# Performance work log

Measured on AMD Instinct MI355X. Metric: run time of the kernel, lower is better.

Reference implementation:

```python
import jax, jax.numpy as jnp
import numpy as np
import math

B, S, D, H = 2, 2048, 1024, 16
D_K = D // H


def setup_inputs() -> dict:
    key = jax.random.key(0)
    ks = jax.random.split(key, 9)
    scale = 0.02
    return {
        "query": jax.random.normal(ks[0], (B, S, D), dtype=jnp.float32),
        "key": jax.random.normal(ks[1], (B, S, D), dtype=jnp.float32),
        "value": jax.random.normal(ks[2], (B, S, D), dtype=jnp.float32),
        "padding_mask": jax.random.bernoulli(ks[3], 0.1, (B, 1, 1, S)),
        "Wq": jax.random.normal(ks[4], (D, D), dtype=jnp.float32) * scale,
        "bq": jnp.zeros((D,), dtype=jnp.float32),
        "Wk": jax.random.normal(ks[5], (D, D), dtype=jnp.float32) * scale,
        "bk": jnp.zeros((D,), dtype=jnp.float32),
        "Wv": jax.random.normal(ks[6], (D, D), dtype=jnp.float32) * scale,
        "bv": jnp.zeros((D,), dtype=jnp.float32),
        "Wo": jax.random.normal(ks[7], (D, D), dtype=jnp.float32) * scale,
        "bo": jnp.zeros((D,), dtype=jnp.float32),
    }


def reference(query, key, value, padding_mask, Wq, bq, Wk, bk, Wv, bv, Wo, bo):
    # projections -> [B, H, S, d_k]
    q = (query @ Wq + bq).reshape(B, S, H, D_K).transpose(0, 2, 1, 3)
    k = (key @ Wk + bk).reshape(B, S, H, D_K).transpose(0, 2, 1, 3)
    v = (value @ Wv + bv).reshape(B, S, H, D_K).transpose(0, 2, 1, 3)

    # scores: [B, H, S, S]
    scores = jnp.einsum("bhqd,bhkd->bhqk", q, k) / math.sqrt(D_K)

    # faithful to original: triu(scores, 1).bool() -> True where upper-tri score != 0,
    # masked positions get value 1e-10 (NOT -inf) before softmax
    causal_mask = jnp.triu(scores, k=1) != 0
    scores = jnp.where(causal_mask, jnp.float32(1e-10), scores)
    scores = jnp.where(padding_mask, jnp.float32(1e-10), scores)

    attn = jax.nn.softmax(scores, axis=-1)
    out = jnp.einsum("bhqk,bhkd->bhqd", attn, v)  # [B, H, S, d_k]
    out = out.transpose(0, 2, 1, 3).reshape(B, S, D)
    return out @ Wo + bo
```

## Files before the change

### kernel.cpp

```cpp
#include <hip/hip_runtime.h>
#include <hip/hip_bf16.h>
#include <cstdint>
#include <cstddef>

typedef __hip_bfloat16 bf16;
typedef __attribute__((ext_vector_type(8))) short short8;
typedef __attribute__((ext_vector_type(4))) short s4v;
typedef __attribute__((ext_vector_type(4))) float floatx4;

#define B_ 2
#define S_ 2048
#define D_ 1024
#define H_ 16
#define DK_ 64
#define M_ 4096
#define HEADELEMS 131072
#define TILEELEMS 4096
#define QSCALE 0.1803368801111204f

struct __align__(8) bf16x4 { bf16 x, y, z, w; };

__device__ __forceinline__ floatx4 mfma16(short8 a, short8 b, floatx4 c) {
  return __builtin_amdgcn_mfma_f32_16x16x32_bf16(a, b, c, 0, 0, 0);
}
__device__ __forceinline__ void gl_lds16(const bf16* g, bf16* l) {
  __builtin_amdgcn_global_load_lds((const __attribute__((address_space(1))) void*)g,
                                   (__attribute__((address_space(3))) void*)l, 16, 0, 0);
}
__device__ __forceinline__ float bs2f(short s) {
  bf16 b = *reinterpret_cast<bf16*>(&s);
  return __bfloat162float(b);
}
__device__ __forceinline__ s4v pack4(float p0, float p1, float p2, float p3) {
  union { __hip_bfloat162 h; short2 s; } ua, ub;
  ua.h = __float22bfloat162_rn(make_float2(p0, p1));
  ub.h = __float22bfloat162_rn(make_float2(p2, p3));
  s4v r = {ua.s.x, ua.s.y, ub.s.x, ub.s.y};
  return r;
}
__device__ __forceinline__ float fast_exp2(float x) {
#if __has_builtin(__builtin_amdgcn_exp2f)
  return __builtin_amdgcn_exp2f(x);
#else
  float r; asm("v_exp_f32 %0, %1" : "=v"(r) : "v"(x)); return r;
#endif
}

__global__ void prep_kernel(const float* __restrict__ q_in, const float* __restrict__ k_in,
                            const float* __restrict__ v_in,
                            const float* __restrict__ Wq, const float* __restrict__ Wk,
                            const float* __restrict__ Wv, const float* __restrict__ Wo,
                            bf16* __restrict__ xq, bf16* __restrict__ xk, bf16* __restrict__ xv,
                            bf16* __restrict__ wqt, bf16* __restrict__ wkt,
                            bf16* __restrict__ wvt, bf16* __restrict__ wot,
                            const unsigned int* __restrict__ pmask, int* __restrict__ flag) {
  __shared__ bf16 tile[64][66];
  __shared__ int sbyte;
  const int blk = blockIdx.x;
  const int tid = threadIdx.x;
  if (blk < 12288) {
    const int z = blk >> 12;
    const int i = ((blk & 4095) << 8) | tid;
    const float* src = (z == 0) ? q_in : (z == 1) ? k_in : v_in;
    bf16* dst = (z == 0) ? xq : (z == 1) ? xk : xv;
    float4 v = ((const float4*)src)[i];
    bf16x4 o = { __float2bfloat16(v.x), __float2bfloat16(v.y),
                 __float2bfloat16(v.z), __float2bfloat16(v.w) };
    ((bf16x4*)dst)[i] = o;
  } else if (blk < 13312) {
    const int t = blk - 12288;
    const int z = t >> 8;
    const int rc = t & 255;
    const int r0 = (rc >> 4) * 64, c0 = (rc & 15) * 64;
    const float* src = (z == 0) ? Wq : (z == 1) ? Wk : (z == 2) ? Wv : Wo;
    bf16* dst = (z == 0) ? wqt : (z == 1) ? wkt : (z == 2) ? wvt : wot;
    const int lr = tid >> 4;
    const int lc4 = (tid & 15) * 4;
#pragma unroll
    for (int i = 0; i < 4; ++i) {
      const int r = lr + i * 16;
      float4 v = *(const float4*)(src + (size_t)(r0 + r) * D_ + c0 + lc4);
      tile[r][lc4 + 0] = __float2bfloat16(v.x);
      tile[r][lc4 + 1] = __float2bfloat16(v.y);
      tile[r][lc4 + 2] = __float2bfloat16(v.z);
      tile[r][lc4 + 3] = __float2bfloat16(v.w);
    }
    __syncthreads();
    const int orr = tid & 63;
    const int oc0 = tid >> 6;
#pragma unroll
    for (int j = 0; j < 16; ++j) {
      const int oc = oc0 + j * 4;
      dst[(size_t)(c0 + oc) * D_ + r0 + orr] = tile[orr][oc];
    }
  } else {
    if (tid == 0) sbyte = 0;
    __syncthreads();
    for (int i = tid; i < (B_ * S_) / 4; i += 256) {
      const unsigned int v = pmask[i];
      if (((v & 0xFEFEFEFEu) == 0u) && ((v & 0xFFFFFF00u) != 0u)) sbyte = 1;
    }
    __syncthreads();
    if (tid == 0) *flag = sbyte;
  }
}

template<int MT>
__global__ __launch_bounds__(256, 2) void gemm_k(
    const bf16* __restrict__ A0, const bf16* __restrict__ A1, const bf16* __restrict__ A2,
    const bf16* __restrict__ W0, const bf16* __restrict__ W1, const bf16* __restrict__ W2,
    const float* __restrict__ b0, const float* __restrict__ b1, const float* __restrict__ b2,
    void* __restrict__ O0, void* __restrict__ O1, void* __restrict__ O2,
    const int mode01, const int Kd, const float sc)
{
  __shared__ __align__(16) bf16 sh[(MT + 128) * 32];
  bf16* As = sh;
  bf16* Bs = sh + MT * 32;
  const int z = blockIdx.z;
  const bf16* A = (z == 0) ? A0 : (z == 1) ? A1 : A2;
  const bf16* W = (z == 0) ? W0 : (z == 1) ? W1 : W2;
  const float* bias = (z == 0) ? b0 : (z == 1) ? b1 : b2;
  void* Cout = (z == 0) ? O0 : (z == 1) ? O1 : O2;
  const int mode = (z == 2) ? 1 : mode01;
  const float scz = (z == 0) ? sc : 1.f;

  constexpr int MI = MT / 32;
  const int tid = threadIdx.x;
  const int wave = tid >> 6, lane = tid & 63;
  const int quad = lane >> 4, lc = lane & 15;
  const int wm = (wave >> 1) * (MT / 2), wn = (wave & 1) * 64;
  const int m0 = blockIdx.y * MT, n0 = blockIdx.x * 128;

  const floatx4 zero4 = {0.f, 0.f, 0.f, 0.f};
  floatx4 acc[MI][4];
#pragma unroll
  for (int mi = 0; mi < MI; ++mi)
#pragma unroll
    for (int ni = 0; ni < 4; ++ni) acc[mi][ni] = zero4;

  const int ldr = lane >> 2;
  const int ldc = (lane & 3) * 8;
  const bf16* Ag = A + (size_t)(m0 + wave * (MT / 4) + ldr) * Kd + ldc;
  const bf16* Bg = W + (size_t)(n0 + wave * 32 + ldr) * Kd + ldc;
  bf16* As0 = As + wave * (MT / 4) * 32;
  bf16* Bs0 = Bs + wave * 32 * 32;

  for (int k0 = 0; k0 < Kd; k0 += 32) {
    gl_lds16(Ag + k0, As0);
    if (MT == 128) gl_lds16(Ag + k0 + (size_t)16 * Kd, As0 + 16 * 32);
    gl_lds16(Bg + k0, Bs0);
    gl_lds16(Bg + k0 + (size_t)16 * Kd, Bs0 + 16 * 32);
    __syncthreads();

    short8 af[MI], bfr[4];
#pragma unroll
    for (int i = 0; i < MI; ++i)
      af[i] = *(const short8*)(As + (wm + i * 16 + lc) * 32 + quad * 8);
#pragma unroll
    for (int i = 0; i < 4; ++i)
      bfr[i] = *(const short8*)(Bs + (wn + i * 16 + lc) * 32 + quad * 8);
#pragma unroll
    for (int mi = 0; mi < MI; ++mi)
#pragma unroll
      for (int ni = 0; ni < 4; ++ni)
        acc[mi][ni] = mfma16(af[mi], bfr[ni], acc[mi][ni]);
    __syncthreads();
  }

  if (mode == 2) {
    float* out = (float*)Cout;
#pragma unroll
    for (int mi = 0; mi < MI; ++mi)
#pragma unroll
      for (int ni = 0; ni < 4; ++ni) {
        const int col = n0 + wn + ni * 16 + lc;
        const float bv = bias[col];
        const int rbase = m0 + wm + mi * 16 + quad * 4;
#pragma unroll
        for (int r = 0; r < 4; ++r)
          out[(size_t)(rbase + r) * D_ + col] = acc[mi][ni][r] + bv;
      }
  } else {
    bf16* pool = sh + wave * 2048;
    float bvs[4];
#pragma unroll
    for (int ni = 0; ni < 4; ++ni) bvs[ni] = bias[n0 + wn + ni * 16 + lc];
    const int hcol = (n0 + wn) >> 6;
    const int mglob = m0 + wm;
    bf16* outb = (bf16*)Cout + (size_t)((mglob >> 11) * H_ + hcol) * HEADELEMS
               + (size_t)((mglob & (S_ - 1)) >> 6) * TILEELEMS;
#pragma unroll
    for (int half = 0; half < MI / 2; ++half) {
#pragma unroll
      for (int mi2 = 0; mi2 < 2; ++mi2) {
        const int mi = half * 2 + mi2;
#pragma unroll
        for (int ni = 0; ni < 4; ++ni) {
          const int dkl = ni * 16 + lc;
#pragma unroll
          for (int r = 0; r < 4; ++r) {
            const float v = (acc[mi][ni][r] + bvs[ni]) * scz;
            int idx;
            if (mode == 0) {
              const int c = (mi2 * 2 + (dkl >> 5)) * 64 + ((dkl >> 3) & 3) * 16 + quad * 4 + r;
              idx = c * 8 + (dkl & 7);
            } else {
              const int c = (mi2 * 4 + (dkl >> 4)) * 64 + quad * 16 + (dkl & 15);
              idx = c * 4 + r;
            }
            pool[idx] = __float2bfloat16(v);
          }
        }
      }
#pragma unroll
      for (int t = 0; t < 4; ++t) {
        const short8 vv = *(const short8*)(pool + t * 512 + lane * 8);
        *(short8*)(outb + half * 2048 + t * 512 + lane * 8) = vv;
      }
    }
  }
}

__global__ void suf_kernel(const bf16* __restrict__ vp, float* __restrict__ suf) {
  __shared__ float ts[32 * 64];
  const int bhid = blockIdx.x;
  const bf16* vb = vp + (size_t)bhid * HEADELEMS;
  const int tid = threadIdx.x;
  const int dk = tid & 63, g = tid >> 6;
  const int dkt = dk >> 4, lck = dk & 15;
  for (int T = g * 8; T < g * 8 + 8; ++T) {
    float sum = 0.f;
#pragma unroll
    for (int w = 0; w < 4; ++w)
#pragma unroll
      for (int qd = 0; qd < 4; ++qd) {
        const s4v x = *(const s4v*)(vb + (size_t)T * TILEELEMS
                                    + (size_t)(((w * 4 + dkt) * 64 + qd * 16 + lck)) * 4);
        sum += bs2f(x[0]) + bs2f(x[1]) + bs2f(x[2]) + bs2f(x[3]);
      }
    ts[T * 64 + dk] = sum;
  }
  __syncthreads();
  if (g == 0) {
    float run = 0.f;
    float* out = suf + (size_t)bhid * (33 * 64);
    out[32 * 64 + dk] = 0.f;
    for (int T = 31; T >= 0; --T) { run += ts[T * 64 + dk]; out[T * 64 + dk] = run; }
  }
}

__device__ __forceinline__ void load_pad(const void* pad, int bytemode, int idx, bool pm[4]) {
  if (bytemode) {
    const uchar4 u = *(const uchar4*)((const unsigned char*)pad + idx);
    pm[0] = u.x != 0; pm[1] = u.y != 0; pm[2] = u.z != 0; pm[3] = u.w != 0;
  } else {
    const int4 u = *(const int4*)((const int*)pad + idx);
    pm[0] = u.x != 0; pm[1] = u.y != 0; pm[2] = u.z != 0; pm[3] = u.w != 0;
  }
}

struct KVF {
  short8 ak00, ak01, ak10, ak11;
  s4v va0[4], va1[4];
  bool pm0[4], pm1[4];
};

__device__ __forceinline__ void load_kv(const bf16* kwp, const bf16* vwp,
                                        const void* pad, const int bytemode,
                                        const int pidx, const int p, KVF& f) {
  const size_t o0 = (size_t)(2 * p) * TILEELEMS, o1 = o0 + TILEELEMS;
  f.ak00 = *(const short8*)(kwp + o0);
  f.ak01 = *(const short8*)(kwp + o0 + 512);
  f.ak10 = *(const short8*)(kwp + o1);
  f.ak11 = *(const short8*)(kwp + o1 + 512);
#pragma unroll
  for (int dkt = 0; dkt < 4; ++dkt) {
    f.va0[dkt] = *(const s4v*)(vwp + o0 + dkt * 256);
    f.va1[dkt] = *(const s4v*)(vwp + o1 + dkt * 256);
  }
  load_pad(pad, bytemode, pidx + 2 * p * 64, f.pm0);
  load_pad(pad, bytemode, pidx + (2 * p + 1) * 64, f.pm1);
}

template<bool DIAGP>
__device__ __forceinline__ void qk_tile(const short8 ak0, const short8 ak1,
                                        const short8 (&qf)[4][2],
                                        const bool pm[4], float (&lacc)[4], s4v (&pf)[4],
                                        const int w, const int quad, const int lc,
                                        const bool diag) {
  const floatx4 z4 = {0.f, 0.f, 0.f, 0.f};
  const short ONE = (short)0x3F80;
#pragma unroll
  for (int qt = 0; qt < 4; ++qt) {
    if (DIAGP && diag && w > qt) {
      s4v o1 = {ONE, ONE, ONE, ONE};
      pf[qt] = o1;
      lacc[qt] += 4.f;
      continue;
    }
    floatx4 s = mfma16(ak0, qf[qt][0], z4);
    s = mfma16(ak1, qf[qt][1], s);
    float pv[4];
#pragma unroll
    for (int r = 0; r < 4; ++r) {
      bool m = pm[r];
      if (DIAGP && diag && w == qt) m = m || (quad * 4 + r > lc);
      pv[r] = fast_exp2(m ? 0.f : s[r]);
      lacc[qt] += pv[r];
    }
    pf[qt] = pack4(pv[0], pv[1], pv[2], pv[3]);
  }
}

__device__ __forceinline__ void pv_step(const KVF& f, const s4v (&pf0)[4], const s4v (&pf1)[4],
                                        floatx4 (&oacc)[4][4]) {
  short8 pB[4];
#pragma unroll
  for (int qt = 0; qt < 4; ++qt)
    pB[qt] = __builtin_shufflevector(pf0[qt], pf1[qt], 0, 1, 2, 3, 4, 5, 6, 7);
#pragma unroll
  for (int dkt = 0; dkt < 4; ++dkt) {
    const short8 av = __builtin_shufflevector(f.va0[dkt], f.va1[dkt], 0, 1, 2, 3, 4, 5, 6, 7);
#pragma unroll
    for (int qt = 0; qt < 4; ++qt)
      oacc[dkt][qt] = mfma16(av, pB[qt], oacc[dkt][qt]);
  }
}

__global__ __launch_bounds__(256, 1) void attn_kernel(
    const bf16* __restrict__ qp, const bf16* __restrict__ kp,
    const bf16* __restrict__ vp, const float* __restrict__ suf,
    const void* __restrict__ pad, const int* __restrict__ flag,
    bf16* __restrict__ oa)
{
  __shared__ __align__(16) bf16 smem[13312];
  __shared__ float lbuf[256];

  const int lin = blockIdx.x;
  const int xcd = lin & 7;
  const int t = lin >> 3;
  const int grp = t >> 4;
  const int jq = t & 15;
  const int bh = xcd + 8 * grp;
  const int b = bh >> 4, h = bh & 15;

  const int tid = threadIdx.x;
  const int w = tid >> 6, lane = tid & 63, quad = lane >> 4, lc = lane & 15;
  const int bytemode = *flag;
  const int pidx = b * S_ + w * 16 + quad * 4;

  const bf16* kwp = kp + (size_t)bh * HEADELEMS + (size_t)(w * 128 + lane) * 8;
  const bf16* vwp = vp + (size_t)bh * HEADELEMS + (size_t)(w * 4 * 64 + lane) * 4;

#pragma unroll 1
  for (int qsel = 0; qsel < 2; ++qsel) {
    const int myqt = qsel ? jq : 31 - jq;
    const int mynt = myqt + 1;
    const int pfull = (mynt - 1) >> 1;

    const bf16* qb = qp + (size_t)bh * HEADELEMS + (size_t)myqt * TILEELEMS;
    short8 qf[4][2];
#pragma unroll
    for (int qt = 0; qt < 4; ++qt)
#pragma unroll
      for (int hh = 0; hh < 2; ++hh)
        qf[qt][hh] = *(const short8*)(qb + (size_t)((qt * 2 + hh) * 64 + lane) * 8);

    const floatx4 zero4 = {0.f, 0.f, 0.f, 0.f};
    floatx4 oacc[4][4];
#pragma unroll
    for (int i = 0; i < 4; ++i)
#pragma unroll
      for (int jj = 0; jj < 4; ++jj) oacc[i][jj] = zero4;
    float lacc[4] = {0.f, 0.f, 0.f, 0.f};

    KVF f;
    load_kv(kwp, vwp, pad, bytemode, pidx, 0, f);
#pragma unroll 1
    for (int p = 0; p < pfull; ++p) {
      KVF fn;
      load_kv(kwp, vwp, pad, bytemode, pidx, p + 1, fn);
      s4v pf0[4], pf1[4];
      qk_tile<false>(f.ak00, f.ak01, qf, f.pm0, lacc, pf0, w, quad, lc, false);
      qk_tile<false>(f.ak10, f.ak11, qf, f.pm1, lacc, pf1, w, quad, lc, false);
      pv_step(f, pf0, pf1, oacc);
      f = fn;
    }
    {
      const int T0 = 2 * pfull, T1 = T0 + 1;
      s4v pf0[4], pf1[4];
      qk_tile<true>(f.ak00, f.ak01, qf, f.pm0, lacc, pf0, w, quad, lc, T0 == mynt - 1);
      if (T1 < mynt) {
        qk_tile<true>(f.ak10, f.ak11, qf, f.pm1, lacc, pf1, w, quad, lc, T1 == mynt - 1);
      } else {
        const s4v zz = {0, 0, 0, 0};
#pragma unroll
        for (int qt = 0; qt < 4; ++qt) pf1[qt] = zz;
      }
      pv_step(f, pf0, pf1, oacc);
    }

#pragma unroll
    for (int qt = 0; qt < 4; ++qt) {
      float v = lacc[qt];
      v += __shfl_xor(v, 16);
      v += __shfl_xor(v, 32);
      if (quad == 0) lbuf[w * 64 + qt * 16 + lc] = v;
    }
    __syncthreads();
    float* fbuf = (float*)smem;
    bf16* obuf = smem + 8704;
    float ls = lbuf[0 * 64 + w * 16 + lc] + lbuf[1 * 64 + w * 16 + lc]
             + lbuf[2 * 64 + w * 16 + lc] + lbuf[3 * 64 + w * 16 + lc];
    ls += (float)(S_ - mynt * 64);
    const float linv = 1.f / ls;
    const float* sufp = suf + (size_t)bh * (33 * 64) + mynt * 64;

#pragma unroll
    for (int dktG = 0; dktG < 4; ++dktG) {
#pragma unroll
      for (int qt = 0; qt < 4; ++qt) {
        const floatx4 a = oacc[dktG][qt];
        float* dst = fbuf + (w * 4 + qt) * 272 + lc;
#pragma unroll
        for (int r = 0; r < 4; ++r) dst[(quad * 4 + r) * 17] = a[r];
      }
      __syncthreads();
      const float4 sv4 = *(const float4*)(sufp + dktG * 16 + quad * 4);
      float v[4];
#pragma unroll
      for (int r = 0; r < 4; ++r) {
        const int e = (quad * 4 + r) * 17 + lc;
        v[r] = fbuf[(0 * 4 + w) * 272 + e] + fbuf[(1 * 4 + w) * 272 + e]
             + fbuf[(2 * 4 + w) * 272 + e] + fbuf[(3 * 4 + w) * 272 + e];
      }
      v[0] = (v[0] + sv4.x) * linv; v[1] = (v[1] + sv4.y) * linv;
      v[2] = (v[2] + sv4.z) * linv; v[3] = (v[3] + sv4.w) * linv;
      bf16x4 pk = { __float2bfloat16(v[0]), __float2bfloat16(v[1]),
                    __float2bfloat16(v[2]), __float2bfloat16(v[3]) };
      *(bf16x4*)(obuf + (w * 16 + lc) * 72 + dktG * 16 + quad * 4) = pk;
      __syncthreads();
    }

    const size_t obase = (size_t)(b * S_ + myqt * 64) * D_ + h * 64;
#pragma unroll
    for (int it = 0; it < 2; ++it) {
      const int idx = it * 256 + tid;
      const int row = idx >> 3, c8 = (idx & 7) * 8;
      const short8 vv = *(const short8*)(obuf + row * 72 + c8);
      *(short8*)(oa + obase + (size_t)row * D_ + c8) = vv;
    }
  }
}

extern "C" void kernel_launch(void* const* d_in, const int* in_sizes, int n_in,
                              void* d_out, int out_size, void* d_ws, size_t ws_size,
                              hipStream_t stream) {
  (void)in_sizes; (void)n_in; (void)out_size; (void)ws_size;
  const float* q_in = (const float*)d_in[0];
  const float* k_in = (const float*)d_in[1];
  const float* v_in = (const float*)d_in[2];
  const void*  pmask = d_in[3];
  const float* Wq = (const float*)d_in[4];
  const float* bq = (const float*)d_in[5];
  const float* Wk = (const float*)d_in[6];
  const float* bk = (const float*)d_in[7];
  const float* Wv = (const float*)d_in[8];
  const float* bv = (const float*)d_in[9];
  const float* Wo = (const float*)d_in[10];
  const float* bo = (const float*)d_in[11];

  char* ws = (char*)d_ws;
  bf16* xq  = (bf16*)(ws + 0);
  bf16* xk  = (bf16*)(ws + 8388608);
  bf16* xv  = (bf16*)(ws + 16777216);
  bf16* wqt = (bf16*)(ws + 25165824);
  bf16* wkt = (bf16*)(ws + 27262976);
  bf16* wvt = (bf16*)(ws + 29360128);
  bf16* wot = (bf16*)(ws + 31457280);
  bf16* qpp = (bf16*)(ws + 33554432);
  bf16* kpp = (bf16*)(ws + 41943040);
  bf16* vpp = (bf16*)(ws + 50331648);
  float* suf = (float*)(ws + 25165824);
  int*  flg = (int*)(ws + 58720256);
  bf16* oa  = xq;

  prep_kernel<<<13313, 256, 0, stream>>>(q_in, k_in, v_in, Wq, Wk, Wv, Wo,
                                         xq, xk, xv, wqt, wkt, wvt, wot,
                                         (const unsigned int*)pmask, flg);

  gemm_k<128><<<dim3(8, 32, 3), 256, 0, stream>>>(xq, xk, xv, wqt, wkt, wvt,
                                                  bq, bk, bv, qpp, kpp, vpp, 0, D_, QSCALE);
  suf_kernel<<<32, 256, 0, stream>>>(vpp, suf);

  attn_kernel<<<512, 256, 0, stream>>>(qpp, kpp, vpp, suf, pmask, flg, oa);

  gemm_k<64><<<dim3(8, 64, 1), 256, 0, stream>>>(oa, oa, oa, wot, wot, wot,
                                                 bo, bo, bo, d_out, d_out, d_out, 2, D_, 1.f);
}
```

Before: 249.7 us.

## Stage K/V tiles through double-buffered LDS with async loads and bitmask padding

Replaces the register-prefetched K/V loads in the attention loop with asynchronous global-to-LDS copies into two ping-pong buffers. Each wave waits only on its own outstanding loads with vmcnt before reading its slice back from LDS. The padding mask is read once per block and packed into per-lane 32-bit masks, so the per-tile mask loads disappear. The goal is to cut register pressure and better hide memory latency. The cost is a larger LDS footprint, extra LDS reads, and extra barriers around the epilogue.

```diff
diff --git a/kernel.cpp b/kernel.cpp
--- a/kernel.cpp
+++ b/kernel.cpp
@@ -249,43 +249,11 @@
   }
 }
 
-__device__ __forceinline__ void load_pad(const void* pad, int bytemode, int idx, bool pm[4]) {
-  if (bytemode) {
-    const uchar4 u = *(const uchar4*)((const unsigned char*)pad + idx);
-    pm[0] = u.x != 0; pm[1] = u.y != 0; pm[2] = u.z != 0; pm[3] = u.w != 0;
-  } else {
-    const int4 u = *(const int4*)((const int*)pad + idx);
-    pm[0] = u.x != 0; pm[1] = u.y != 0; pm[2] = u.z != 0; pm[3] = u.w != 0;
-  }
-}
-
-struct KVF {
-  short8 ak00, ak01, ak10, ak11;
-  s4v va0[4], va1[4];
-  bool pm0[4], pm1[4];
-};
-
-__device__ __forceinline__ void load_kv(const bf16* kwp, const bf16* vwp,
-                                        const void* pad, const int bytemode,
-                                        const int pidx, const int p, KVF& f) {
-  const size_t o0 = (size_t)(2 * p) * TILEELEMS, o1 = o0 + TILEELEMS;
-  f.ak00 = *(const short8*)(kwp + o0);
-  f.ak01 = *(const short8*)(kwp + o0 + 512);
-  f.ak10 = *(const short8*)(kwp + o1);
-  f.ak11 = *(const short8*)(kwp + o1 + 512);
-#pragma unroll
-  for (int dkt = 0; dkt < 4; ++dkt) {
-    f.va0[dkt] = *(const s4v*)(vwp + o0 + dkt * 256);
-    f.va1[dkt] = *(const s4v*)(vwp + o1 + dkt * 256);
-  }
-  load_pad(pad, bytemode, pidx + 2 * p * 64, f.pm0);
-  load_pad(pad, bytemode, pidx + (2 * p + 1) * 64, f.pm1);
-}
-
 template<bool DIAGP>
 __device__ __forceinline__ void qk_tile(const short8 ak0, const short8 ak1,
                                         const short8 (&qf)[4][2],
-                                        const bool pm[4], float (&lacc)[4], s4v (&pf)[4],
+                                        const unsigned int (&pmb)[4], const int T,
+                                        float (&lacc)[4], s4v (&pf)[4],
                                         const int w, const int quad, const int lc,
                                         const bool diag) {
   const floatx4 z4 = {0.f, 0.f, 0.f, 0.f};
@@ -303,7 +271,7 @@
     float pv[4];
 #pragma unroll
     for (int r = 0; r < 4; ++r) {
-      bool m = pm[r];
+      bool m = ((pmb[r] >> T) & 1u) != 0u;
       if (DIAGP && diag && w == qt) m = m || (quad * 4 + r > lc);
       pv[r] = fast_exp2(m ? 0.f : s[r]);
       lacc[qt] += pv[r];
@@ -312,7 +280,8 @@
   }
 }
 
-__device__ __forceinline__ void pv_step(const KVF& f, const s4v (&pf0)[4], const s4v (&pf1)[4],
+__device__ __forceinline__ void pv_step(const s4v (&va0)[4], const s4v (&va1)[4],
+                                        const s4v (&pf0)[4], const s4v (&pf1)[4],
                                         floatx4 (&oacc)[4][4]) {
   short8 pB[4];
 #pragma unroll
@@ -320,11 +289,28 @@
     pB[qt] = __builtin_shufflevector(pf0[qt], pf1[qt], 0, 1, 2, 3, 4, 5, 6, 7);
 #pragma unroll
   for (int dkt = 0; dkt < 4; ++dkt) {
-    const short8 av = __builtin_shufflevector(f.va0[dkt], f.va1[dkt], 0, 1, 2, 3, 4, 5, 6, 7);
+    const short8 av = __builtin_shufflevector(va0[dkt], va1[dkt], 0, 1, 2, 3, 4, 5, 6, 7);
 #pragma unroll
     for (int qt = 0; qt < 4; ++qt)
       oacc[dkt][qt] = mfma16(av, pB[qt], oacc[dkt][qt]);
   }
+}
+
+__device__ __forceinline__ void stage8(const bf16* kb, const bf16* vb, bf16* slot,
+                                       const int T0, const int T1,
+                                       const int wl, const int wreg) {
+  const bf16* k0 = kb + (size_t)T0 * TILEELEMS + wl;
+  const bf16* k1 = kb + (size_t)T1 * TILEELEMS + wl;
+  const bf16* v0 = vb + (size_t)T0 * TILEELEMS + wl;
+  const bf16* v1 = vb + (size_t)T1 * TILEELEMS + wl;
+  gl_lds16(k0,       slot + wreg);
+  gl_lds16(k0 + 512, slot + wreg + 512);
+  gl_lds16(k1,       slot + 4096 + wreg);
+  gl_lds16(k1 + 512, slot + 4096 + wreg + 512);
+  gl_lds16(v0,       slot + 8192 + wreg);
+  gl_lds16(v0 + 512, slot + 8192 + wreg + 512);
+  gl_lds16(v1,       slot + 12288 + wreg);
+  gl_lds16(v1 + 512, slot + 12288 + wreg + 512);
 }
 
 __global__ __launch_bounds__(256, 1) void attn_kernel(
@@ -333,8 +319,7 @@
     const void* __restrict__ pad, const int* __restrict__ flag,
     bf16* __restrict__ oa)
 {
-  __shared__ __align__(16) bf16 smem[13312];
-  __shared__ float lbuf[256];
+  __shared__ __align__(16) bf16 lds[32768];
 
   const int lin = blockIdx.x;
   const int xcd = lin & 7;
@@ -347,24 +332,57 @@
   const int tid = threadIdx.x;
   const int w = tid >> 6, lane = tid & 63, quad = lane >> 4, lc = lane & 15;
   const int bytemode = *flag;
-  const int pidx = b * S_ + w * 16 + quad * 4;
-
-  const bf16* kwp = kp + (size_t)bh * HEADELEMS + (size_t)(w * 128 + lane) * 8;
-  const bf16* vwp = vp + (size_t)bh * HEADELEMS + (size_t)(w * 4 * 64 + lane) * 4;
+
+  const int wreg = w * 1024;
+  const int wl = wreg + lane * 8;
+  const int vl = wreg + lane * 4;
+
+  const bf16* kb = kp + (size_t)bh * HEADELEMS;
+  const bf16* vb = vp + (size_t)bh * HEADELEMS;
+
+  unsigned int pmb[4] = {0u, 0u, 0u, 0u};
+  if (bytemode) {
+    const unsigned char* pp = (const unsigned char*)pad + b * S_ + w * 16 + quad * 4;
+#pragma unroll
+    for (int T = 0; T < 32; ++T) {
+      const uchar4 u = *(const uchar4*)(pp + T * 64);
+      pmb[0] |= (u.x ? 1u : 0u) << T;
+      pmb[1] |= (u.y ? 1u : 0u) << T;
+      pmb[2] |= (u.z ? 1u : 0u) << T;
+      pmb[3] |= (u.w ? 1u : 0u) << T;
+    }
+  } else {
+    const int* pp = (const int*)pad + b * S_ + w * 16 + quad * 4;
+#pragma unroll
+    for (int T = 0; T < 32; ++T) {
+      const int4 u = *(const int4*)(pp + (size_t)T * 64);
+      pmb[0] |= (u.x ? 1u : 0u) << T;
+      pmb[1] |= (u.y ? 1u : 0u) << T;
+      pmb[2] |= (u.z ? 1u : 0u) << T;
+      pmb[3] |= (u.w ? 1u : 0u) << T;
+    }
+  }
 
 #pragma unroll 1
   for (int qsel = 0; qsel < 2; ++qsel) {
     const int myqt = qsel ? jq : 31 - jq;
     const int mynt = myqt + 1;
-    const int pfull = (mynt - 1) >> 1;
+    const int np = (mynt + 1) >> 1;
 
     const bf16* qb = qp + (size_t)bh * HEADELEMS + (size_t)myqt * TILEELEMS;
+    gl_lds16(qb + wl,       lds + 16384 + wreg);
+    gl_lds16(qb + wl + 512, lds + 16384 + wreg + 512);
+    stage8(kb, vb, lds, 0, 1, wl, wreg);
+    asm volatile("s_waitcnt vmcnt(0)" ::: "memory");
+    __syncthreads();
+
     short8 qf[4][2];
 #pragma unroll
     for (int qt = 0; qt < 4; ++qt)
 #pragma unroll
       for (int hh = 0; hh < 2; ++hh)
-        qf[qt][hh] = *(const short8*)(qb + (size_t)((qt * 2 + hh) * 64 + lane) * 8);
+        qf[qt][hh] = *(const short8*)(lds + 16384 + qt * 1024 + hh * 512 + lane * 8);
+    __syncthreads();
 
     const floatx4 zero4 = {0.f, 0.f, 0.f, 0.f};
     floatx4 oacc[4][4];
@@ -374,31 +392,51 @@
       for (int jj = 0; jj < 4; ++jj) oacc[i][jj] = zero4;
     float lacc[4] = {0.f, 0.f, 0.f, 0.f};
 
-    KVF f;
-    load_kv(kwp, vwp, pad, bytemode, pidx, 0, f);
 #pragma unroll 1
-    for (int p = 0; p < pfull; ++p) {
-      KVF fn;
-      load_kv(kwp, vwp, pad, bytemode, pidx, p + 1, fn);
+    for (int p = 0; p < np; ++p) {
+      if (p + 1 < np) {
+        stage8(kb, vb, lds + (((p + 1) & 1) << 14), 2 * p + 2, 2 * p + 3, wl, wreg);
+        asm volatile("s_waitcnt vmcnt(8)" ::: "memory");
+      } else {
+        asm volatile("s_waitcnt vmcnt(0)" ::: "memory");
+      }
+      __builtin_amdgcn_sched_barrier(0);
+
+      bf16* slot = lds + ((p & 1) << 14);
+      const short8 ak00 = *(const short8*)(slot + wl);
+      const short8 ak01 = *(const short8*)(slot + wl + 512);
+      const short8 ak10 = *(const short8*)(slot + 4096 + wl);
+      const short8 ak11 = *(const short8*)(slot + 4096 + wl + 512);
+      s4v va0[4], va1[4];
+#pragma unroll
+      for (int dkt = 0; dkt < 4; ++dkt) {
+        va0[dkt] = *(const s4v*)(slot + 8192 + vl + dkt * 256);
+        va1[dkt] = *(const s4v*)(slot + 12288 + vl + dkt * 256);
+      }
+
+      const int T0 = 2 * p, T1 = 2 * p + 1;
       s4v pf0[4], pf1[4];
-      qk_tile<false>(f.ak00, f.ak01, qf, f.pm0, lacc, pf0, w, quad, lc, false);
-      qk_tile<false>(f.ak10, f.ak11, qf, f.pm1, lacc, pf1, w, quad, lc, false);
-      pv_step(f, pf0, pf1, oacc);
-      f = fn;
-    }
-    {
-      const int T0 = 2 * pfull, T1 = T0 + 1;
-      s4v pf0[4], pf1[4];
-      qk_tile<true>(f.ak00, f.ak01, qf, f.pm0, lacc, pf0, w, quad, lc, T0 == mynt - 1);
-      if (T1 < mynt) {
-        qk_tile<true>(f.ak10, f.ak11, qf, f.pm1, lacc, pf1, w, quad, lc, T1 == mynt - 1);
+      if (p + 1 < np) {
+        qk_tile<false>(ak00, ak01, qf, pmb, T0, lacc, pf0, w, quad, lc, false);
+        qk_tile<false>(ak10, ak11, qf, pmb, T1, lacc, pf1, w, quad, lc, false);
       } else {
-        const s4v zz = {0, 0, 0, 0};
-#pragma unroll
-        for (int qt = 0; qt < 4; ++qt) pf1[qt] = zz;
-      }
-      pv_step(f, pf0, pf1, oacc);
-    }
+        qk_tile<true>(ak00, ak01, qf, pmb, T0, lacc, pf0, w, quad, lc, T0 == mynt - 1);
+        if (T1 < mynt) {
+          qk_tile<true>(ak10, ak11, qf, pmb, T1, lacc, pf1, w, quad, lc, true);
+        } else {
+          const s4v zz = {0, 0, 0, 0};
+#pragma unroll
+          for (int qt = 0; qt < 4; ++qt) pf1[qt] = zz;
+        }
+      }
+      pv_step(va0, va1, pf0, pf1, oacc);
+    }
+
+    __syncthreads();
+
+    float* fbuf = (float*)lds;
+    bf16* obuf = lds + 8704;
+    float* lbuf = (float*)(lds + 13312);
 
 #pragma unroll
     for (int qt = 0; qt < 4; ++qt) {
@@ -408,8 +446,6 @@
       if (quad == 0) lbuf[w * 64 + qt * 16 + lc] = v;
     }
     __syncthreads();
-    float* fbuf = (float*)smem;
-    bf16* obuf = smem + 8704;
     float ls = lbuf[0 * 64 + w * 16 + lc] + lbuf[1 * 64 + w * 16 + lc]
              + lbuf[2 * 64 + w * 16 + lc] + lbuf[3 * 64 + w * 16 + lc];
     ls += (float)(S_ - mynt * 64);
@@ -450,6 +486,7 @@
       const short8 vv = *(const short8*)(obuf + row * 72 + c8);
       *(short8*)(oa + obase + (size_t)row * D_ + c8) = vv;
     }
+    __syncthreads();
   }
 }
 
```

Result: faster. 222.7 us (-10.8%).
